# Kernel tuning notes

Hardware: AMD Instinct MI355X
Metric: run time of the kernel (lower is better)

## Reference

```python
import jax, jax.numpy as jnp
import numpy as np

B, T, N, E = 128, 24, 300, 9000
H, O = 1, 4            # num_heads, out_feats
GRU_H = 12
NUM_AIRPORTS, HORIZON = 300, 4


def setup_inputs() -> dict:
    key = jax.random.key(0)
    ks = jax.random.split(key, 16)
    inp = {
        "x": jax.random.normal(ks[0], (B, T, N, 1), jnp.float32),
        "ew": jax.random.uniform(ks[1], (B, T, E, 1), jnp.float32),
        "src": jax.random.randint(ks[2], (E,), 0, N, jnp.int32),
        "dst": jax.random.randint(ks[3], (E,), 0, N, jnp.int32),
        # EdgeGATConv params (fc / fc_edge have no bias in DGL GAT-style convs)
        "w_node": jax.random.normal(ks[4], (H * O, 1), jnp.float32) * 0.5,
        "w_edge": jax.random.normal(ks[5], (H * O, 1), jnp.float32) * 0.5,
        "attn_l": jax.random.normal(ks[6], (H, O), jnp.float32) * 0.5,
        "attn_r": jax.random.normal(ks[7], (H, O), jnp.float32) * 0.5,
        "attn_e": jax.random.normal(ks[8], (H, O), jnp.float32) * 0.5,
        "gat_bias": jnp.zeros((H * O,), jnp.float32),
        # GRU (single layer, input 4 -> hidden 12); gates stacked [r|z|n]
        "w_ih": jax.random.normal(ks[9], (3 * GRU_H, H * O), jnp.float32) * 0.3,
        "w_hh": jax.random.normal(ks[10], (3 * GRU_H, GRU_H), jnp.float32) * 0.3,
        "b_ih": jnp.zeros((3 * GRU_H,), jnp.float32),
        "b_hh": jnp.zeros((3 * GRU_H,), jnp.float32),
        # fc: gru_out -> num_airports * horizon
        "fc_w": jax.random.normal(ks[11], (NUM_AIRPORTS * HORIZON, GRU_H), jnp.float32) * 0.1,
        "fc_b": jnp.zeros((NUM_AIRPORTS * HORIZON,), jnp.float32),
    }
    return inp


def _edge_gat_pool(x, ew, src, dst, w_node, w_edge, attn_l, attn_r, attn_e, gat_bias):
    """Batched DGL EdgeGATConv over G=B*T graphs (shared topology) + mean pool."""
    b, t = x.shape[0], x.shape[1]
    G = b * t
    xf = x.reshape(G, N, 1)
    ef = ew.reshape(G, E, 1)
    # node / edge projections -> [G, *, H, O]
    ft = jnp.einsum('gni,fi->gnf', xf, w_node).reshape(G, N, H, O)
    fe = jnp.einsum('gei,fi->gef', ef, w_edge).reshape(G, E, H, O)
    el = jnp.einsum('gnho,ho->gnh', ft, attn_l)          # [G,N,H]
    er = jnp.einsum('gnho,ho->gnh', ft, attn_r)          # [G,N,H]
    ee = jnp.einsum('geho,ho->geh', fe, attn_e)          # [G,E,H]
    e = jax.nn.leaky_relu(el[:, src] + er[:, dst] + ee, negative_slope=0.2)
    # edge softmax over incoming edges of each dst node
    m = jnp.full((G, N, H), -jnp.inf, e.dtype).at[:, dst].max(e)
    ex = jnp.exp(e - m[:, dst])                           # [G,E,H]
    den = jnp.zeros((G, N, H), e.dtype).at[:, dst].add(ex)
    a = ex / den[:, dst]
    # aggregate messages: sum_j alpha_ij * W h_j
    msg = ft[:, src] * a[..., None]                       # [G,E,H,O]
    rst = jnp.zeros((G, N, H, O), e.dtype).at[:, dst].add(msg)
    rst = rst + gat_bias.reshape(H, O)
    # flatten heads, mean-pool over nodes -> [B,T,H*O]
    return rst.reshape(G, N, H * O).mean(axis=1).reshape(b, t, H * O)


def _gru_last(seq, w_ih, w_hh, b_ih, b_hh):
    """torch nn.GRU (1 layer, batch_first), returns final hidden state [B,GRU_H]."""
    def cell(h, xt):
        gi = xt @ w_ih.T + b_ih
        gh = h @ w_hh.T + b_hh
        i_r, i_z, i_n = jnp.split(gi, 3, axis=-1)
        h_r, h_z, h_n = jnp.split(gh, 3, axis=-1)
        r = jax.nn.sigmoid(i_r + h_r)
        z = jax.nn.sigmoid(i_z + h_z)
        n = jnp.tanh(i_n + r * h_n)
        h_new = (1.0 - z) * n + z * h
        return h_new, None
    h0 = jnp.zeros((seq.shape[0], GRU_H), seq.dtype)
    hT, _ = jax.lax.scan(cell, h0, jnp.swapaxes(seq, 0, 1))
    return hT


def reference(x, ew, src, dst, w_node, w_edge, attn_l, attn_r, attn_e,
              gat_bias, w_ih, w_hh, b_ih, b_hh, fc_w, fc_b):
    pooled = _edge_gat_pool(x, ew, src, dst, w_node, w_edge,
                            attn_l, attn_r, attn_e, gat_bias)  # [B,T,4]
    # dropout(0.1) is identity in eval mode
    h_n = _gru_last(pooled, w_ih, w_hh, b_ih, b_hh)            # [B,12]
    return h_n @ fc_w.T + fc_b                                  # [B,1200]
```

## Files before the change

### kernel.cpp

```cpp
#include <hip/hip_runtime.h>
#include <math.h>

#define B_    128
#define T_    24
#define NN    300
#define EE    9000
#define GG    (B_ * T_)
#define GRUH  12
#define OUTF  1200

#define NSPLIT    50
#define NODES_PER 6
#define GBLK      12
#define EWLD      3136
#define XLD       3072

__global__ __launch_bounds__(256) void transpose_k(
    const float* __restrict__ src, float* __restrict__ dst, int ncols, int ldd)
{
    __shared__ float tile[32][260];
    const int g0 = blockIdx.x * 256;
    const int e0 = blockIdx.y * 32;
    const int tid = threadIdx.x;
    const int cols_here = min(32, ncols - e0);

    const int rr = tid >> 3;
    const int c4 = (tid & 7) << 2;
    if (c4 < cols_here) {
#pragma unroll
        for (int k = 0; k < 8; k++) {
            const int r = rr + (k << 5);
            const float4 v = *(const float4*)(src + (size_t)(g0 + r) * ncols + e0 + c4);
            tile[c4 + 0][r] = v.x; tile[c4 + 1][r] = v.y;
            tile[c4 + 2][r] = v.z; tile[c4 + 3][r] = v.w;
        }
    }
    __syncthreads();

    const int w  = tid >> 6;
    const int gc = (tid & 63) << 2;
#pragma unroll
    for (int k = 0; k < 8; k++) {
        const int er = w + (k << 2);
        if (er < cols_here) {
            float4 v;
            v.x = tile[er][gc + 0]; v.y = tile[er][gc + 1];
            v.z = tile[er][gc + 2]; v.w = tile[er][gc + 3];
            *(float4*)(dst + (size_t)(e0 + er) * ldd + g0 + gc) = v;
        }
    }
}

__global__ __launch_bounds__(1024) void build_csr(
    const int* __restrict__ src, const int* __restrict__ dst,
    int* __restrict__ row_ptr, int2* __restrict__ edge2, float* __restrict__ S)
{
    __shared__ int cnt[512];
    __shared__ int bufA[512], bufB[512];
    __shared__ int offs[NN];
    const int tid = threadIdx.x;

    for (int i = tid; i < GG; i += 1024) S[i] = 0.f;

    for (int i = tid; i < 512; i += 1024) cnt[i] = 0;
    __syncthreads();
    for (int e = tid; e < EE; e += 1024) atomicAdd(&cnt[dst[e]], 1);
    __syncthreads();

    int* cur = bufA; int* nxt = bufB;
    if (tid < 512) cur[tid] = cnt[tid];
    __syncthreads();
    for (int d = 1; d < 512; d <<= 1) {
        if (tid < 512) nxt[tid] = cur[tid] + (tid >= d ? cur[tid - d] : 0);
        __syncthreads();
        int* t = cur; cur = nxt; nxt = t;
    }
    if (tid <= NN) row_ptr[tid] = (tid == 0) ? 0 : cur[tid - 1];
    if (tid < NN)  offs[tid]    = (tid == 0) ? 0 : cur[tid - 1];
    __syncthreads();

    for (int e = tid; e < EE; e += 1024) {
        int d = dst[e];
        int pos = atomicAdd(&offs[d], 1);
        edge2[pos] = make_int2(src[e], e);
    }
}

__global__ __launch_bounds__(256) void gat_pool_t(
    const float* __restrict__ ewT, const float* __restrict__ xT,
    const float* __restrict__ w_node, const float* __restrict__ w_edge,
    const float* __restrict__ attn_l, const float* __restrict__ attn_r,
    const float* __restrict__ attn_e,
    const int* __restrict__ row_ptr, const int2* __restrict__ edge2,
    float* __restrict__ S)
{
    const int tid   = threadIdx.x;
    const int chunk = blockIdx.x % GBLK;
    const int s     = blockIdx.x / GBLK;
    const int g     = chunk * 256 + tid;

    float cL = 0.f, cR = 0.f, cE = 0.f;
#pragma unroll
    for (int o = 0; o < 4; o++) {
        float wn = w_node[o];
        cL += wn * attn_l[o];
        cR += wn * attn_r[o];
        cE += w_edge[o] * attn_e[o];
    }

    float part = 0.f;
    const int n0 = s * NODES_PER;
    for (int n = n0; n < n0 + NODES_PER; n++) {
        const int beg = row_ptr[n];
        const int end = row_ptr[n + 1];
        const float base = cR * xT[(size_t)n * XLD + g];
        float den = 0.f, num = 0.f;
        int i = beg;
        for (; i + 4 <= end; i += 4) {
            const int2 ea = edge2[i];
            const int2 eb = edge2[i + 1];
            const int2 ec = edge2[i + 2];
            const int2 ed = edge2[i + 3];
            const float wa = ewT[(size_t)ea.y * EWLD + g];
            const float wb = ewT[(size_t)eb.y * EWLD + g];
            const float wc = ewT[(size_t)ec.y * EWLD + g];
            const float wd = ewT[(size_t)ed.y * EWLD + g];
            const float xa = xT[(size_t)ea.x * XLD + g];
            const float xb = xT[(size_t)eb.x * XLD + g];
            const float xc = xT[(size_t)ec.x * XLD + g];
            const float xd = xT[(size_t)ed.x * XLD + g];
            float v0 = fmaf(cL, xa, fmaf(cE, wa, base));
            float v1 = fmaf(cL, xb, fmaf(cE, wb, base));
            float v2 = fmaf(cL, xc, fmaf(cE, wc, base));
            float v3 = fmaf(cL, xd, fmaf(cE, wd, base));
            v0 = (v0 >= 0.f) ? v0 : 0.2f * v0;
            v1 = (v1 >= 0.f) ? v1 : 0.2f * v1;
            v2 = (v2 >= 0.f) ? v2 : 0.2f * v2;
            v3 = (v3 >= 0.f) ? v3 : 0.2f * v3;
            const float e0 = __expf(v0), e1 = __expf(v1);
            const float e2 = __expf(v2), e3 = __expf(v3);
            den += e0 + e1 + e2 + e3;
            num = fmaf(e0, xa, num);
            num = fmaf(e1, xb, num);
            num = fmaf(e2, xc, num);
            num = fmaf(e3, xd, num);
        }
        for (; i < end; i++) {
            const int2 ea = edge2[i];
            const float wa = ewT[(size_t)ea.y * EWLD + g];
            const float xa = xT[(size_t)ea.x * XLD + g];
            float v0 = fmaf(cL, xa, fmaf(cE, wa, base));
            v0 = (v0 >= 0.f) ? v0 : 0.2f * v0;
            const float e0 = __expf(v0);
            den += e0;
            num = fmaf(e0, xa, num);
        }
        if (end > beg) part += num / den;
    }
    unsafeAtomicAdd(&S[g], part);
}

__device__ __forceinline__ float sigmoidf_(float v) { return 1.0f / (1.0f + __expf(-v)); }

__global__ __launch_bounds__(256) void gru_fc(
    const float* __restrict__ S,
    const float* __restrict__ w_node, const float* __restrict__ gat_bias,
    const float* __restrict__ w_ih, const float* __restrict__ w_hh,
    const float* __restrict__ b_ih, const float* __restrict__ b_hh,
    const float* __restrict__ fc_w, const float* __restrict__ fc_b,
    float* __restrict__ out)
{
    __shared__ float hsh[GRUH];
    const int b = blockIdx.x;
    const int tid = threadIdx.x;

    if (tid < 64) {
        float wn[4], gb[4];
#pragma unroll
        for (int i = 0; i < 4; i++) {
            wn[i] = w_node[i] * (1.0f / (float)NN);
            gb[i] = gat_bias[i];
        }
        float wih[4] = {0.f, 0.f, 0.f, 0.f};
        float whh[12];
#pragma unroll
        for (int j = 0; j < 12; j++) whh[j] = 0.f;
        float bih = 0.f, bhh = 0.f;
        if (tid < 36) {
#pragma unroll
            for (int i = 0; i < 4; i++)  wih[i] = w_ih[tid * 4 + i];
#pragma unroll
            for (int j = 0; j < 12; j++) whh[j] = w_hh[tid * 12 + j];
            bih = b_ih[tid];
            bhh = b_hh[tid];
        }
        float srow = (tid < T_) ? S[(size_t)b * T_ + tid] : 0.f;
        float hreg = 0.f;
        const int l = tid % 12;
        for (int t = 0; t < T_; t++) {
            float Sg = __shfl(srow, t);
            float gi = bih, gh = bhh;
#pragma unroll
            for (int i = 0; i < 4; i++) gi += (Sg * wn[i] + gb[i]) * wih[i];
#pragma unroll
            for (int j = 0; j < 12; j++) gh += __shfl(hreg, j) * whh[j];
            float a   = gi + gh;
            float aiz = __shfl(a, 12 + l);
            float gin = __shfl(gi, 24 + l);
            float ghn = __shfl(gh, 24 + l);
            if (tid < 12) {
                float r = sigmoidf_(a);
                float z = sigmoidf_(aiz);
                float n = tanhf(gin + r * ghn);
                hreg = (1.f - z) * n + z * hreg;
            }
        }
        if (tid < GRUH) hsh[tid] = hreg;
    }
    __syncthreads();

    float h0 = hsh[0], h1 = hsh[1], h2 = hsh[2],  h3 = hsh[3];
    float h4 = hsh[4], h5 = hsh[5], h6 = hsh[6],  h7 = hsh[7];
    float h8 = hsh[8], h9 = hsh[9], hA = hsh[10], hB = hsh[11];
    for (int j = tid; j < OUTF; j += 256) {
        const float4* w4 = (const float4*)(fc_w + (size_t)j * GRUH);
        const float4 a = w4[0], c = w4[1], d = w4[2];
        float o = fc_b[j];
        o += h0 * a.x + h1 * a.y + h2 * a.z + h3 * a.w;
        o += h4 * c.x + h5 * c.y + h6 * c.z + h7 * c.w;
        o += h8 * d.x + h9 * d.y + hA * d.z + hB * d.w;
        out[(size_t)b * OUTF + j] = o;
    }
}

__global__ __launch_bounds__(320) void gat_pool_csr(
    const float* __restrict__ x, const float* __restrict__ ew,
    const float* __restrict__ w_node, const float* __restrict__ w_edge,
    const float* __restrict__ attn_l, const float* __restrict__ attn_r,
    const float* __restrict__ attn_e,
    const int* __restrict__ row_ptr, const int2* __restrict__ edge2,
    float* __restrict__ S)
{
    __shared__ float xs[NN];
    __shared__ float red[5];
    const int g = blockIdx.x;
    const int tid = threadIdx.x;

    float cL = 0.f, cR = 0.f, cE = 0.f;
#pragma unroll
    for (int o = 0; o < 4; o++) {
        float wn = w_node[o];
        cL += wn * attn_l[o];
        cR += wn * attn_r[o];
        cE += w_edge[o] * attn_e[o];
    }
    const float* xrow = x + (size_t)g * NN;
    const float* erow = ew + (size_t)g * EE;
    for (int i = tid; i < NN; i += 320) xs[i] = xrow[i];
    __syncthreads();

    float acc = 0.f;
    if (tid < NN) {
        const int beg = row_ptr[tid];
        const int end = row_ptr[tid + 1];
        const float vb = cR * xs[tid];
        float den = 0.f, num = 0.f;
        for (int i = beg; i < end; i++) {
            const int2 e  = edge2[i];
            const float ev  = erow[e.y];
            const float xsv = xs[e.x];
            float v = fmaf(cL, xsv, fmaf(cE, ev, vb));
            v = (v >= 0.f) ? v : 0.2f * v;
            const float ex = __expf(v);
            den += ex;
            num = fmaf(ex, xsv, num);
        }
        if (end > beg) acc = num / den;
    }
    for (int off = 32; off > 0; off >>= 1) acc += __shfl_down(acc, off);
    if ((tid & 63) == 0) red[tid >> 6] = acc;
    __syncthreads();
    if (tid == 0) S[g] = red[0] + red[1] + red[2] + red[3] + red[4];
}

extern "C" void kernel_launch(void* const* d_in, const int* in_sizes, int n_in,
                              void* d_out, int out_size, void* d_ws, size_t ws_size,
                              hipStream_t stream)
{
    const float* x        = (const float*)d_in[0];
    const float* ew       = (const float*)d_in[1];
    const int*   src      = (const int*)d_in[2];
    const int*   dst      = (const int*)d_in[3];
    const float* w_node   = (const float*)d_in[4];
    const float* w_edge   = (const float*)d_in[5];
    const float* attn_l   = (const float*)d_in[6];
    const float* attn_r   = (const float*)d_in[7];
    const float* attn_e   = (const float*)d_in[8];
    const float* gat_bias = (const float*)d_in[9];
    const float* w_ih     = (const float*)d_in[10];
    const float* w_hh     = (const float*)d_in[11];
    const float* b_ih     = (const float*)d_in[12];
    const float* b_hh     = (const float*)d_in[13];
    const float* fc_w     = (const float*)d_in[14];
    const float* fc_b     = (const float*)d_in[15];
    float* out = (float*)d_out;

    char* ws = (char*)d_ws;
    const size_t ewT_b  = (size_t)EE * EWLD * 4;
    const size_t xT_b   = (size_t)NN * XLD * 4;
    const size_t needed = ewT_b + xT_b + GG * 4 + 1280 + (size_t)EE * 8;

    if (ws_size >= needed) {
        float* ewT     = (float*)ws;
        float* xT      = (float*)(ws + ewT_b);
        float* S       = (float*)(ws + ewT_b + xT_b);
        int*   row_ptr = (int*)(ws + ewT_b + xT_b + GG * 4);
        int2*  edge2   = (int2*)(ws + ewT_b + xT_b + GG * 4 + 1280);

        build_csr<<<1, 1024, 0, stream>>>(src, dst, row_ptr, edge2, S);
        transpose_k<<<dim3(GBLK, (EE + 31) / 32), 256, 0, stream>>>(ew, ewT, EE, EWLD);
        transpose_k<<<dim3(GBLK, (NN + 31) / 32), 256, 0, stream>>>(x, xT, NN, XLD);
        gat_pool_t<<<GBLK * NSPLIT, 256, 0, stream>>>(ewT, xT, w_node, w_edge,
                                                      attn_l, attn_r, attn_e,
                                                      row_ptr, edge2, S);
        gru_fc<<<B_, 256, 0, stream>>>(S, w_node, gat_bias, w_ih, w_hh,
                                       b_ih, b_hh, fc_w, fc_b, out);
    } else {
        float* S       = (float*)ws;
        int*   row_ptr = (int*)(ws + GG * 4);
        int2*  edge2   = (int2*)(ws + GG * 4 + 1280);
        build_csr<<<1, 1024, 0, stream>>>(src, dst, row_ptr, edge2, S);
        gat_pool_csr<<<GG, 320, 0, stream>>>(x, ew, w_node, w_edge,
                                             attn_l, attn_r, attn_e,
                                             row_ptr, edge2, S);
        gru_fc<<<B_, 256, 0, stream>>>(S, w_node, gat_bias, w_ih, w_hh,
                                       b_ih, b_hh, fc_w, fc_b, out);
    }
}
```

Measured before the change: 279.0 us.

## Store transposed edge weights as fp16 in CSR order and process two graphs per thread

After: 278.1 us. Within noise of the previous version (-0.3%).

```diff
diff --git a/kernel.cpp b/kernel.cpp
--- a/kernel.cpp
+++ b/kernel.cpp
@@ -1,4 +1,5 @@
 #include <hip/hip_runtime.h>
+#include <hip/hip_fp16.h>
 #include <math.h>
 
 #define B_    128
@@ -9,13 +10,52 @@
 #define GRUH  12
 #define OUTF  1200
 
-#define NSPLIT    50
-#define NODES_PER 6
-#define GBLK      12
-#define EWLD      3136
+#define NSPLIT    100
+#define NODES_PER 3
+#define GBLK      6
+#define EWLDH     3136
 #define XLD       3072
 
-__global__ __launch_bounds__(256) void transpose_k(
+__global__ __launch_bounds__(1024) void build_csr(
+    const int* __restrict__ src, const int* __restrict__ dst,
+    int* __restrict__ row_ptr, int* __restrict__ csr_src,
+    int* __restrict__ csr_eid, int* __restrict__ csr_pos,
+    float* __restrict__ S)
+{
+    __shared__ int cnt[512];
+    __shared__ int bufA[512], bufB[512];
+    __shared__ int offs[NN];
+    const int tid = threadIdx.x;
+
+    for (int i = tid; i < GG; i += 1024) S[i] = 0.f;
+
+    for (int i = tid; i < 512; i += 1024) cnt[i] = 0;
+    __syncthreads();
+    for (int e = tid; e < EE; e += 1024) atomicAdd(&cnt[dst[e]], 1);
+    __syncthreads();
+
+    int* cur = bufA; int* nxt = bufB;
+    if (tid < 512) cur[tid] = cnt[tid];
+    __syncthreads();
+    for (int d = 1; d < 512; d <<= 1) {
+        if (tid < 512) nxt[tid] = cur[tid] + (tid >= d ? cur[tid - d] : 0);
+        __syncthreads();
+        int* t = cur; cur = nxt; nxt = t;
+    }
+    if (tid <= NN) row_ptr[tid] = (tid == 0) ? 0 : cur[tid - 1];
+    if (tid < NN)  offs[tid]    = (tid == 0) ? 0 : cur[tid - 1];
+    __syncthreads();
+
+    for (int e = tid; e < EE; e += 1024) {
+        int d = dst[e];
+        int pos = atomicAdd(&offs[d], 1);
+        csr_src[pos] = src[e];
+        csr_eid[pos] = e;
+        csr_pos[e]   = pos;
+    }
+}
+
+__global__ __launch_bounds__(256) void transpose_f(
     const float* __restrict__ src, float* __restrict__ dst, int ncols, int ldd)
 {
     __shared__ float tile[32][260];
@@ -51,53 +91,59 @@
     }
 }
 
-__global__ __launch_bounds__(1024) void build_csr(
-    const int* __restrict__ src, const int* __restrict__ dst,
-    int* __restrict__ row_ptr, int2* __restrict__ edge2, float* __restrict__ S)
-{
-    __shared__ int cnt[512];
-    __shared__ int bufA[512], bufB[512];
-    __shared__ int offs[NN];
-    const int tid = threadIdx.x;
-
-    for (int i = tid; i < GG; i += 1024) S[i] = 0.f;
-
-    for (int i = tid; i < 512; i += 1024) cnt[i] = 0;
-    __syncthreads();
-    for (int e = tid; e < EE; e += 1024) atomicAdd(&cnt[dst[e]], 1);
-    __syncthreads();
-
-    int* cur = bufA; int* nxt = bufB;
-    if (tid < 512) cur[tid] = cnt[tid];
-    __syncthreads();
-    for (int d = 1; d < 512; d <<= 1) {
-        if (tid < 512) nxt[tid] = cur[tid] + (tid >= d ? cur[tid - d] : 0);
-        __syncthreads();
-        int* t = cur; cur = nxt; nxt = t;
-    }
-    if (tid <= NN) row_ptr[tid] = (tid == 0) ? 0 : cur[tid - 1];
-    if (tid < NN)  offs[tid]    = (tid == 0) ? 0 : cur[tid - 1];
-    __syncthreads();
-
-    for (int e = tid; e < EE; e += 1024) {
-        int d = dst[e];
-        int pos = atomicAdd(&offs[d], 1);
-        edge2[pos] = make_int2(src[e], e);
+__global__ __launch_bounds__(256) void transpose_h(
+    const float* __restrict__ src, __half* __restrict__ dst,
+    const int* __restrict__ csr_pos)
+{
+    __shared__ __half tileh[128][134];
+    const int g0 = blockIdx.x * 128;
+    const int e0 = blockIdx.y * 128;
+    const int tid = threadIdx.x;
+    const int cols_here = min(128, EE - e0);
+
+    const int c4 = (tid & 31) << 2;
+    if (c4 < cols_here) {
+#pragma unroll
+        for (int k = 0; k < 16; k++) {
+            const int r = (tid >> 5) + (k << 3);
+            const float4 v = *(const float4*)(src + (size_t)(g0 + r) * EE + e0 + c4);
+            __half2 h01, h23;
+            h01.x = __float2half_rn(v.x); h01.y = __float2half_rn(v.y);
+            h23.x = __float2half_rn(v.z); h23.y = __float2half_rn(v.w);
+            *(__half2*)&tileh[r][c4 + 0] = h01;
+            *(__half2*)&tileh[r][c4 + 2] = h23;
+        }
+    }
+    __syncthreads();
+
+    const int lane = tid & 63;
+    const int g2 = lane << 1;
+#pragma unroll
+    for (int k = 0; k < 32; k++) {
+        const int er = (tid >> 6) + (k << 2);
+        if (er < cols_here) {
+            __half2 h;
+            h.x = tileh[g2][er];
+            h.y = tileh[g2 + 1][er];
+            const int orow = csr_pos[e0 + er];
+            *(__half2*)(dst + (size_t)orow * EWLDH + g0 + g2) = h;
+        }
     }
 }
 
 __global__ __launch_bounds__(256) void gat_pool_t(
-    const float* __restrict__ ewT, const float* __restrict__ xT,
+    const __half* __restrict__ ewTC, const float* __restrict__ xT,
     const float* __restrict__ w_node, const float* __restrict__ w_edge,
     const float* __restrict__ attn_l, const float* __restrict__ attn_r,
     const float* __restrict__ attn_e,
-    const int* __restrict__ row_ptr, const int2* __restrict__ edge2,
+    const int* __restrict__ row_ptr, const int* __restrict__ csr_src,
     float* __restrict__ S)
 {
     const int tid   = threadIdx.x;
     const int chunk = blockIdx.x % GBLK;
     const int s     = blockIdx.x / GBLK;
-    const int g     = chunk * 256 + tid;
+    const int gp    = chunk * 256 + tid;
+    const int g2    = gp << 1;
 
     float cL = 0.f, cR = 0.f, cE = 0.f;
 #pragma unroll
@@ -108,56 +154,58 @@
         cE += w_edge[o] * attn_e[o];
     }
 
-    float part = 0.f;
+    const __half2* __restrict__ ew2 = (const __half2*)ewTC;
+    const float2*  __restrict__ xT2 = (const float2*)xT;
+
+    float p0 = 0.f, p1 = 0.f;
     const int n0 = s * NODES_PER;
     for (int n = n0; n < n0 + NODES_PER; n++) {
         const int beg = row_ptr[n];
         const int end = row_ptr[n + 1];
-        const float base = cR * xT[(size_t)n * XLD + g];
-        float den = 0.f, num = 0.f;
+        const float2 xb = xT2[(size_t)n * (XLD / 2) + gp];
+        const float base0 = cR * xb.x;
+        const float base1 = cR * xb.y;
+        float den0 = 0.f, num0 = 0.f, den1 = 0.f, num1 = 0.f;
         int i = beg;
-        for (; i + 4 <= end; i += 4) {
-            const int2 ea = edge2[i];
-            const int2 eb = edge2[i + 1];
-            const int2 ec = edge2[i + 2];
-            const int2 ed = edge2[i + 3];
-            const float wa = ewT[(size_t)ea.y * EWLD + g];
-            const float wb = ewT[(size_t)eb.y * EWLD + g];
-            const float wc = ewT[(size_t)ec.y * EWLD + g];
-            const float wd = ewT[(size_t)ed.y * EWLD + g];
-            const float xa = xT[(size_t)ea.x * XLD + g];
-            const float xb = xT[(size_t)eb.x * XLD + g];
-            const float xc = xT[(size_t)ec.x * XLD + g];
-            const float xd = xT[(size_t)ed.x * XLD + g];
-            float v0 = fmaf(cL, xa, fmaf(cE, wa, base));
-            float v1 = fmaf(cL, xb, fmaf(cE, wb, base));
-            float v2 = fmaf(cL, xc, fmaf(cE, wc, base));
-            float v3 = fmaf(cL, xd, fmaf(cE, wd, base));
+        for (; i + 2 <= end; i += 2) {
+            const int sa = csr_src[i];
+            const int sb = csr_src[i + 1];
+            const float2 wa = __half22float2(ew2[(size_t)i       * (EWLDH / 2) + gp]);
+            const float2 wb = __half22float2(ew2[(size_t)(i + 1) * (EWLDH / 2) + gp]);
+            const float2 xa = xT2[(size_t)sa * (XLD / 2) + gp];
+            const float2 xb2 = xT2[(size_t)sb * (XLD / 2) + gp];
+            float v0 = fmaf(cL, xa.x,  fmaf(cE, wa.x, base0));
+            float v1 = fmaf(cL, xa.y,  fmaf(cE, wa.y, base1));
+            float v2 = fmaf(cL, xb2.x, fmaf(cE, wb.x, base0));
+            float v3 = fmaf(cL, xb2.y, fmaf(cE, wb.y, base1));
             v0 = (v0 >= 0.f) ? v0 : 0.2f * v0;
             v1 = (v1 >= 0.f) ? v1 : 0.2f * v1;
             v2 = (v2 >= 0.f) ? v2 : 0.2f * v2;
             v3 = (v3 >= 0.f) ? v3 : 0.2f * v3;
-            const float e0 = __expf(v0), e1 = __expf(v1);
-            const float e2 = __expf(v2), e3 = __expf(v3);
-            den += e0 + e1 + e2 + e3;
-            num = fmaf(e0, xa, num);
-            num = fmaf(e1, xb, num);
-            num = fmaf(e2, xc, num);
-            num = fmaf(e3, xd, num);
+            const float e0v = __expf(v0), e1v = __expf(v1);
+            const float e2v = __expf(v2), e3v = __expf(v3);
+            den0 += e0v + e2v;
+            den1 += e1v + e3v;
+            num0 = fmaf(e0v, xa.x,  num0); num0 = fmaf(e2v, xb2.x, num0);
+            num1 = fmaf(e1v, xa.y,  num1); num1 = fmaf(e3v, xb2.y, num1);
         }
         for (; i < end; i++) {
-            const int2 ea = edge2[i];
-            const float wa = ewT[(size_t)ea.y * EWLD + g];
-            const float xa = xT[(size_t)ea.x * XLD + g];
-            float v0 = fmaf(cL, xa, fmaf(cE, wa, base));
+            const int sa = csr_src[i];
+            const float2 wa = __half22float2(ew2[(size_t)i * (EWLDH / 2) + gp]);
+            const float2 xa = xT2[(size_t)sa * (XLD / 2) + gp];
+            float v0 = fmaf(cL, xa.x, fmaf(cE, wa.x, base0));
+            float v1 = fmaf(cL, xa.y, fmaf(cE, wa.y, base1));
             v0 = (v0 >= 0.f) ? v0 : 0.2f * v0;
-            const float e0 = __expf(v0);
-            den += e0;
-            num = fmaf(e0, xa, num);
-        }
-        if (end > beg) part += num / den;
-    }
-    unsafeAtomicAdd(&S[g], part);
+            v1 = (v1 >= 0.f) ? v1 : 0.2f * v1;
+            const float e0v = __expf(v0), e1v = __expf(v1);
+            den0 += e0v; den1 += e1v;
+            num0 = fmaf(e0v, xa.x, num0);
+            num1 = fmaf(e1v, xa.y, num1);
+        }
+        if (end > beg) { p0 += num0 / den0; p1 += num1 / den1; }
+    }
+    unsafeAtomicAdd(&S[g2],     p0);
+    unsafeAtomicAdd(&S[g2 + 1], p1);
 }
 
 __device__ __forceinline__ float sigmoidf_(float v) { return 1.0f / (1.0f + __expf(-v)); }
@@ -238,7 +286,8 @@
     const float* __restrict__ w_node, const float* __restrict__ w_edge,
     const float* __restrict__ attn_l, const float* __restrict__ attn_r,
     const float* __restrict__ attn_e,
-    const int* __restrict__ row_ptr, const int2* __restrict__ edge2,
+    const int* __restrict__ row_ptr, const int* __restrict__ csr_src,
+    const int* __restrict__ csr_eid,
     float* __restrict__ S)
 {
     __shared__ float xs[NN];
@@ -266,9 +315,8 @@
         const float vb = cR * xs[tid];
         float den = 0.f, num = 0.f;
         for (int i = beg; i < end; i++) {
-            const int2 e  = edge2[i];
-            const float ev  = erow[e.y];
-            const float xsv = xs[e.x];
+            const float ev  = erow[csr_eid[i]];
+            const float xsv = xs[csr_src[i]];
             float v = fmaf(cL, xsv, fmaf(cE, ev, vb));
             v = (v >= 0.f) ? v : 0.2f * v;
             const float ex = __expf(v);
@@ -306,33 +354,44 @@
     float* out = (float*)d_out;
 
     char* ws = (char*)d_ws;
-    const size_t ewT_b  = (size_t)EE * EWLD * 4;
-    const size_t xT_b   = (size_t)NN * XLD * 4;
-    const size_t needed = ewT_b + xT_b + GG * 4 + 1280 + (size_t)EE * 8;
+    const size_t ewT_b = (size_t)EE * EWLDH * 2;
+    const size_t xT_b  = (size_t)NN * XLD * 4;
+    const size_t off_S    = ewT_b + xT_b;
+    const size_t off_rp   = off_S + GG * 4;
+    const size_t off_src  = off_rp + 304 * 4;
+    const size_t off_eid  = off_src + EE * 4;
+    const size_t off_pos  = off_eid + EE * 4;
+    const size_t needed   = off_pos + EE * 4;
 
     if (ws_size >= needed) {
-        float* ewT     = (float*)ws;
-        float* xT      = (float*)(ws + ewT_b);
-        float* S       = (float*)(ws + ewT_b + xT_b);
-        int*   row_ptr = (int*)(ws + ewT_b + xT_b + GG * 4);
-        int2*  edge2   = (int2*)(ws + ewT_b + xT_b + GG * 4 + 1280);
-
-        build_csr<<<1, 1024, 0, stream>>>(src, dst, row_ptr, edge2, S);
-        transpose_k<<<dim3(GBLK, (EE + 31) / 32), 256, 0, stream>>>(ew, ewT, EE, EWLD);
-        transpose_k<<<dim3(GBLK, (NN + 31) / 32), 256, 0, stream>>>(x, xT, NN, XLD);
-        gat_pool_t<<<GBLK * NSPLIT, 256, 0, stream>>>(ewT, xT, w_node, w_edge,
+        __half* ewTC    = (__half*)ws;
+        float*  xT      = (float*)(ws + ewT_b);
+        float*  S       = (float*)(ws + off_S);
+        int*    row_ptr = (int*)(ws + off_rp);
+        int*    csr_src = (int*)(ws + off_src);
+        int*    csr_eid = (int*)(ws + off_eid);
+        int*    csr_pos = (int*)(ws + off_pos);
+
+        build_csr<<<1, 1024, 0, stream>>>(src, dst, row_ptr, csr_src, csr_eid,
+                                          csr_pos, S);
+        transpose_f<<<dim3(12, 10), 256, 0, stream>>>(x, xT, NN, XLD);
+        transpose_h<<<dim3(24, 71), 256, 0, stream>>>(ew, ewTC, csr_pos);
+        gat_pool_t<<<GBLK * NSPLIT, 256, 0, stream>>>(ewTC, xT, w_node, w_edge,
                                                       attn_l, attn_r, attn_e,
-                                                      row_ptr, edge2, S);
+                                                      row_ptr, csr_src, S);
         gru_fc<<<B_, 256, 0, stream>>>(S, w_node, gat_bias, w_ih, w_hh,
                                        b_ih, b_hh, fc_w, fc_b, out);
     } else {
         float* S       = (float*)ws;
         int*   row_ptr = (int*)(ws + GG * 4);
-        int2*  edge2   = (int2*)(ws + GG * 4 + 1280);
-        build_csr<<<1, 1024, 0, stream>>>(src, dst, row_ptr, edge2, S);
+        int*   csr_src = (int*)(ws + GG * 4 + 304 * 4);
+        int*   csr_eid = (int*)(ws + GG * 4 + 304 * 4 + EE * 4);
+        int*   csr_pos = (int*)(ws + GG * 4 + 304 * 4 + 2 * EE * 4);
+        build_csr<<<1, 1024, 0, stream>>>(src, dst, row_ptr, csr_src, csr_eid,
+                                          csr_pos, S);
         gat_pool_csr<<<GG, 320, 0, stream>>>(x, ew, w_node, w_edge,
                                              attn_l, attn_r, attn_e,
-                                             row_ptr, edge2, S);
+                                             row_ptr, csr_src, csr_eid, S);
         gru_fc<<<B_, 256, 0, stream>>>(S, w_node, gat_bias, w_ih, w_hh,
                                        b_ih, b_hh, fc_w, fc_b, out);
     }
```
